# Kernel tuning notes

Measured on AMD Instinct MI355X. Metric: run time of the kernel, lower is better.

Reference implementation:

```python
import jax, jax.numpy as jnp
import numpy as np

L = 10
DIM = 4
TABLE = 1 << 16
BASE_RES = 16.0
PLS = 2.0
HID = 64
SCALE_MULTI = 0.5
DENSITY_OFFSET = -1.0
SCENE_SCALING = 2.0
PRIMES = (np.uint32(1), np.uint32(2654435761), np.uint32(805459861))


def _safe_exp(x):
    return jnp.exp(jnp.clip(x, -30.0, 10.0))


def _l2norm(x, eps=1e-8):
    return x / jnp.sqrt(jnp.sum(x * x, -1, keepdims=True) + eps)


def _circumcenters(tets):
    # tets: [T,4,3]; solve 2(vi-v0).c = |vi|^2-|v0|^2
    v0 = tets[:, 0]
    A = 2.0 * (tets[:, 1:] - v0[:, None, :]) + 1e-6 * jnp.eye(3, dtype=tets.dtype)
    b = jnp.sum(tets[:, 1:] ** 2, -1) - jnp.sum(v0 ** 2, -1)[:, None]
    c = jnp.linalg.solve(A, b[..., None])[..., 0]
    r = jnp.linalg.norm(c - v0, axis=-1)
    return c, r


def _project_to_tet(p, tets):
    # clamp-and-renormalize barycentric coordinates (approximate projection)
    v0 = tets[:, 0]
    E = tets[:, 1:] - v0[:, None, :]
    M = jnp.einsum('tid,tjd->tij', E, E) + 1e-6 * jnp.eye(3, dtype=tets.dtype)
    rhs = jnp.einsum('tid,td->ti', E, p - v0)
    lam = jnp.linalg.solve(M, rhs[..., None])[..., 0]
    bary = jnp.concatenate([1.0 - lam.sum(-1, keepdims=True), lam], -1)
    bary = jnp.clip(bary, 0.0, 1.0)
    bary = bary / jnp.clip(bary.sum(-1, keepdims=True), 1e-6, None)
    return jnp.einsum('tv,tvd->td', bary, tets)


def _contract_mean_std(x, std):
    # mipnerf-360 style scene contraction of mean; std scaled by |J| ~ 1/n^2
    n = jnp.maximum(jnp.linalg.norm(x, axis=-1, keepdims=True), 1e-9)
    cx = jnp.where(n <= 1.0, x, (2.0 - 1.0 / n) * x / n)
    cs = std * jnp.where(n[..., 0] <= 1.0, 1.0, 1.0 / (n[..., 0] ** 2))
    return cx, cs


def _hash_encode(pos, tables):
    # pos [T,3] in [0,1); tables [L, TABLE, DIM]; multiresolution hash grid
    mask = np.uint32(TABLE - 1)
    pos = jnp.clip(pos, 0.0, 1.0 - 1e-6)
    feats = []
    for l in range(L):
        res = float(np.floor(BASE_RES * (PLS ** l)))
        x = pos * res
        f = jnp.floor(x)
        w = x - f
        fi = f.astype(jnp.uint32)
        acc = jnp.zeros(pos.shape[:-1] + (DIM,), pos.dtype)
        for cz in (0, 1):
            for cy in (0, 1):
                for cx in (0, 1):
                    c = fi + jnp.asarray((cx, cy, cz), jnp.uint32)
                    h = ((c[..., 0] * PRIMES[0]) ^ (c[..., 1] * PRIMES[1]) ^ (c[..., 2] * PRIMES[2])) & mask
                    wt = ((w[..., 0] if cx else 1.0 - w[..., 0]) *
                          (w[..., 1] if cy else 1.0 - w[..., 1]) *
                          (w[..., 2] if cz else 1.0 - w[..., 2]))
                    acc = acc + tables[l][h.astype(jnp.int32)] * wt[..., None]
        feats.append(acc)
    return jnp.stack(feats, axis=1)  # [T, L, DIM]


def _forward(vertices, indices, center, tables, W1, b1, W2, b2, W3, b3):
    tets = vertices[indices]  # [T,4,3] gather
    cc, radius = _circumcenters(tets)
    cc = _project_to_tet(cc, tets)
    normalized = (cc - center) / SCENE_SCALING
    cv, cr = _contract_mean_std(normalized, radius / SCENE_SCALING)
    cr = cr * SCALE_MULTI
    n = jnp.arange(L, dtype=vertices.dtype)
    erf_x = 1.0 / jnp.sqrt(PLS * 4.0 * n[None, :] * cr[:, None] + 1e-12)
    scaling = jax.lax.erf(erf_x)  # [T, L] per-level erf anti-aliasing scale
    pos = cv * 0.25 + 0.5  # contracted [-2,2] -> [0,1]
    feats = _hash_encode(pos, tables) * scaling[..., None]
    h = feats.reshape(feats.shape[0], L * DIM)
    h = jax.nn.selu(h @ W1 + b1)
    h = jax.nn.selu(h @ W2 + b2)
    out = h @ W3 + b3  # [T, 13]
    density = _safe_exp(out[:, 0] + DENSITY_OFFSET)
    pairs = ((0, 1), (0, 2), (0, 3), (1, 2), (1, 3), (2, 3))
    el = jnp.stack([jnp.linalg.norm(tets[:, i] - tets[:, j], axis=1) for i, j in pairs], 0).max(0)
    alpha = 1.0 - jnp.exp(-density * el)
    V = vertices.shape[0]
    vertex_alpha = jnp.zeros((V,), vertices.dtype).at[indices].max(
        jnp.broadcast_to(alpha[:, None], indices.shape))  # scatter amax
    fs = out[:, 1:]
    base = fs[:, :3] + 0.5
    grads = jnp.clip(base[:, :, None], 0.0, None) * jnp.tanh(fs[:, 3:12].reshape(-1, 3, 3))
    offs = _l2norm(tets - cc[:, None, :])
    vcol = base[:, None, :] + jnp.einsum('tcd,tvd->tvc', grads, offs)  # [T,4,3]
    return vertex_alpha, vcol


def setup_inputs() -> dict:
    key = jax.random.key(0)
    ks = jax.random.split(key, 8)
    V, T = 100000, 500000
    vertices = jax.random.normal(ks[0], (V, 3), jnp.float32) * 0.5
    indices = jax.random.randint(ks[1], (T, 4), 0, V, jnp.int32)
    center = jnp.zeros((1, 3), jnp.float32)
    tables = jax.random.normal(ks[2], (L, TABLE, DIM), jnp.float32) * 1e-2
    def lin(k, i, o):
        s = (6.0 / (i + o)) ** 0.5
        return jax.random.uniform(k, (i, o), jnp.float32, -s, s)
    return dict(vertices=vertices, indices=indices, center=center, tables=tables,
                W1=lin(ks[3], L * DIM, HID), b1=jnp.zeros((HID,), jnp.float32),
                W2=lin(ks[4], HID, HID), b2=jnp.zeros((HID,), jnp.float32),
                W3=lin(ks[5], HID, 13), b3=jnp.zeros((13,), jnp.float32))


def reference(vertices, indices, center, tables, W1, b1, W2, b2, W3, b3):
    return _forward(vertices, indices, center, tables, W1, b1, W2, b2, W3, b3)
```

## Files before the change

kernel.cpp:

```cpp
#include <hip/hip_runtime.h>
#include <math.h>

#define NLVL 10
#define TBL 65536
#define NHID 64
#define NIN 40
#define LDP 68

typedef __attribute__((ext_vector_type(8))) short bf16x8;
typedef __attribute__((ext_vector_type(4))) float f32x4;
typedef unsigned int uint;

__device__ __forceinline__ float selu_f(float x) {
    return 1.0507009873554805f * (x > 0.0f ? x : 1.6732632423543772f * (__expf(x) - 1.0f));
}
__device__ __forceinline__ float fast_tanh(float x) {
    float xx = fminf(fmaxf(x, -15.0f), 15.0f);
    float t = __expf(2.0f * xx);
    return (t - 1.0f) / (t + 1.0f);
}
__device__ __forceinline__ unsigned short f2bf(float x) {
    unsigned u = __float_as_uint(x);
    unsigned r = (u + 0x7FFFu + ((u >> 16) & 1u)) >> 16;
    return (unsigned short)r;
}
__device__ __forceinline__ float bf2f(unsigned short h) {
    return __uint_as_float(((unsigned)h) << 16);
}
__device__ __forceinline__ short2 split_bf(float x) {
    unsigned short h = f2bf(x);
    float r = x - bf2f(h);
    short2 s;
    s.x = (short)h;
    s.y = (short)f2bf(r);
    return s;
}

__device__ __forceinline__ void solve3d(const double A[3][3], const double b[3], double x[3]) {
    double a00=A[0][0], a01=A[0][1], a02=A[0][2];
    double a10=A[1][0], a11=A[1][1], a12=A[1][2];
    double a20=A[2][0], a21=A[2][1], a22=A[2][2];
    double C00 =  (a11*a22 - a12*a21);
    double C01 = -(a10*a22 - a12*a20);
    double C02 =  (a10*a21 - a11*a20);
    double C10 = -(a01*a22 - a02*a21);
    double C11 =  (a00*a22 - a02*a20);
    double C12 = -(a00*a21 - a01*a20);
    double C20 =  (a01*a12 - a02*a11);
    double C21 = -(a00*a12 - a02*a10);
    double C22 =  (a00*a11 - a01*a10);
    double det = a00*C00 + a01*C01 + a02*C02;
    double inv = 1.0 / det;
    x[0] = (C00*b[0] + C10*b[1] + C20*b[2]) * inv;
    x[1] = (C01*b[0] + C11*b[1] + C21*b[2]) * inv;
    x[2] = (C02*b[0] + C12*b[1] + C22*b[2]) * inv;
}

__global__ void __launch_bounds__(256) zero_alpha_kernel(float* out, int V) {
    int i = blockIdx.x * blockDim.x + threadIdx.x;
    if (i < V) out[i] = 0.0f;
}

__device__ __forceinline__ void enc2(const float4* __restrict__ tb4,
                                     float px, float py, float pz, float crf,
                                     int l0, float f[8]) {
    uint idx[2][8];
    float wt[2][8];
    #pragma unroll
    for (int h = 0; h < 2; ++h) {
        int l = l0 + h;
        float res = (float)(16 << l);
        float x0 = px*res, x1 = py*res, x2 = pz*res;
        float f0 = floorf(x0), f1 = floorf(x1), f2 = floorf(x2);
        float w0 = x0-f0, w1 = x1-f1, w2 = x2-f2;
        uint i0 = (uint)f0, i1 = (uint)f1, i2 = (uint)f2;
        #pragma unroll
        for (int cn = 0; cn < 8; ++cn) {
            uint cx = (uint)(cn & 1), cy = (uint)((cn >> 1) & 1), cz = (uint)((cn >> 2) & 1);
            idx[h][cn] = (((i0 + cx) * 1u) ^ ((i1 + cy) * 2654435761u) ^ ((i2 + cz) * 805459861u)) & 65535u;
            wt[h][cn] = (cx ? w0 : 1.0f - w0) * (cy ? w1 : 1.0f - w1) * (cz ? w2 : 1.0f - w2);
        }
    }
    float4 v[2][8];
    #pragma unroll
    for (int h = 0; h < 2; ++h)
        #pragma unroll
        for (int cn = 0; cn < 8; ++cn)
            v[h][cn] = tb4[(size_t)(l0+h)*TBL + idx[h][cn]];
    #pragma unroll
    for (int h = 0; h < 2; ++h) {
        float a0=0.f, a1=0.f, a2=0.f, a3=0.f;
        #pragma unroll
        for (int cn = 0; cn < 8; ++cn) {
            float w = wt[h][cn];
            a0 = fmaf(v[h][cn].x, w, a0);
            a1 = fmaf(v[h][cn].y, w, a1);
            a2 = fmaf(v[h][cn].z, w, a2);
            a3 = fmaf(v[h][cn].w, w, a3);
        }
        float sc = erff(rsqrtf(8.0f*(float)(l0+h)*crf + 1e-12f));
        f[h*4+0] = a0*sc; f[h*4+1] = a1*sc; f[h*4+2] = a2*sc; f[h*4+3] = a3*sc;
    }
}

__global__ void __launch_bounds__(256) geomhash_kernel(
    const float* __restrict__ vertices,
    const int*   __restrict__ indices,
    const float* __restrict__ center,
    const float* __restrict__ tables,
    float* __restrict__ aux,
    float* __restrict__ feats, int T)
{
    int t = blockIdx.x * blockDim.x + threadIdx.x;
    if (t >= T) return;

    double p[4][3];
    #pragma unroll
    for (int v = 0; v < 4; ++v) {
        int vid = indices[t*4+v];
        p[v][0] = (double)vertices[vid*3+0];
        p[v][1] = (double)vertices[vid*3+1];
        p[v][2] = (double)vertices[vid*3+2];
    }

    double A[3][3], bb[3];
    double v0sq = p[0][0]*p[0][0] + p[0][1]*p[0][1] + p[0][2]*p[0][2];
    #pragma unroll
    for (int i = 0; i < 3; ++i) {
        #pragma unroll
        for (int j = 0; j < 3; ++j)
            A[i][j] = 2.0*(p[i+1][j] - p[0][j]) + (i==j ? 1e-6 : 0.0);
        bb[i] = p[i+1][0]*p[i+1][0] + p[i+1][1]*p[i+1][1] + p[i+1][2]*p[i+1][2] - v0sq;
    }
    double c[3];
    solve3d(A, bb, c);
    double dx0 = c[0]-p[0][0], dy0 = c[1]-p[0][1], dz0 = c[2]-p[0][2];
    double radius = sqrt(dx0*dx0 + dy0*dy0 + dz0*dz0);

    double E[3][3];
    #pragma unroll
    for (int i = 0; i < 3; ++i)
        #pragma unroll
        for (int j = 0; j < 3; ++j)
            E[i][j] = p[i+1][j] - p[0][j];
    double M[3][3], rhs[3];
    #pragma unroll
    for (int i = 0; i < 3; ++i) {
        #pragma unroll
        for (int k = 0; k < 3; ++k)
            M[i][k] = E[i][0]*E[k][0] + E[i][1]*E[k][1] + E[i][2]*E[k][2] + (i==k ? 1e-6 : 0.0);
        rhs[i] = E[i][0]*dx0 + E[i][1]*dy0 + E[i][2]*dz0;
    }
    double lam[3];
    solve3d(M, rhs, lam);
    double bary[4];
    bary[0] = 1.0 - lam[0] - lam[1] - lam[2];
    bary[1] = lam[0]; bary[2] = lam[1]; bary[3] = lam[2];
    double bs = 0.0;
    #pragma unroll
    for (int v = 0; v < 4; ++v) {
        bary[v] = fmin(fmax(bary[v], 0.0), 1.0);
        bs += bary[v];
    }
    bs = fmax(bs, 1e-6);
    double cc[3];
    #pragma unroll
    for (int j = 0; j < 3; ++j)
        cc[j] = (bary[0]*p[0][j] + bary[1]*p[1][j] + bary[2]*p[2][j] + bary[3]*p[3][j]) / bs;

    double xv[3];
    xv[0] = (cc[0] - (double)center[0]) * 0.5;
    xv[1] = (cc[1] - (double)center[1]) * 0.5;
    xv[2] = (cc[2] - (double)center[2]) * 0.5;
    double nrm = sqrt(xv[0]*xv[0] + xv[1]*xv[1] + xv[2]*xv[2]);
    double n = fmax(nrm, 1e-9);
    double cv[3], cs;
    if (n <= 1.0) {
        cv[0]=xv[0]; cv[1]=xv[1]; cv[2]=xv[2];
        cs = radius * 0.5;
    } else {
        double f = (2.0 - 1.0/n) / n;
        cv[0]=xv[0]*f; cv[1]=xv[1]*f; cv[2]=xv[2]*f;
        cs = radius * 0.5 / (n*n);
    }
    float crf = (float)(cs * 0.5);

    float px = fminf(fmaxf((float)(cv[0]*0.25 + 0.5), 0.0f), 1.0f - 1e-6f);
    float py = fminf(fmaxf((float)(cv[1]*0.25 + 0.5), 0.0f), 1.0f - 1e-6f);
    float pz = fminf(fmaxf((float)(cv[2]*0.25 + 0.5), 0.0f), 1.0f - 1e-6f);

    float el = 0.0f;
    #pragma unroll
    for (int a = 0; a < 3; ++a)
        #pragma unroll
        for (int bq = a+1; bq < 4; ++bq) {
            float ddx = (float)(p[a][0]-p[bq][0]);
            float ddy = (float)(p[a][1]-p[bq][1]);
            float ddz = (float)(p[a][2]-p[bq][2]);
            el = fmaxf(el, sqrtf(ddx*ddx + ddy*ddy + ddz*ddz));
        }

    size_t st = (size_t)T;
    aux[4*st + t] = (float)cc[0];
    aux[5*st + t] = (float)cc[1];
    aux[6*st + t] = (float)cc[2];
    aux[7*st + t] = el;

    const float4* tb4 = reinterpret_cast<const float4*>(tables);
    float4* frow = reinterpret_cast<float4*>(feats + (size_t)t * NIN);
    #pragma unroll
    for (int b = 0; b < 5; ++b) {
        float f[8];
        enc2(tb4, px, py, pz, crf, 2*b, f);
        frow[2*b+0] = make_float4(f[0], f[1], f[2], f[3]);
        frow[2*b+1] = make_float4(f[4], f[5], f[6], f[7]);
    }
}

__global__ void __launch_bounds__(256, 2) mlp_mfma_kernel(
    const float* __restrict__ feats,
    const float* __restrict__ aux,
    const float* __restrict__ vertices,
    const int*   __restrict__ indices,
    const float* __restrict__ W1, const float* __restrict__ b1,
    const float* __restrict__ W2, const float* __restrict__ b2,
    const float* __restrict__ W3, const float* __restrict__ b3,
    float* __restrict__ out, int T, int V)
{
    __shared__ __align__(16) float hts[4][16][LDP];

    const int tid  = threadIdx.x;
    const int wid  = tid >> 6;
    const int lane = tid & 63;
    const int r    = lane & 15;
    const int g    = lane >> 4;

    bf16x8 w1h[2][4];
    bf16x8 w1l0[4];
    #pragma unroll
    for (int s = 0; s < 2; ++s)
        #pragma unroll
        for (int nt = 0; nt < 4; ++nt) {
            bf16x8 h, lo;
            #pragma unroll
            for (int j = 0; j < 8; ++j) {
                int k = s*32 + g*8 + j;
                float w = (k < NIN) ? W1[k*NHID + nt*16 + r] : 0.0f;
                short2 sp = split_bf(w);
                h[j] = sp.x; lo[j] = sp.y;
            }
            w1h[s][nt] = h;
            if (s == 0) w1l0[nt] = lo;
        }
    bf16x8 w2h[2][4], w2l[2][4];
    #pragma unroll
    for (int s = 0; s < 2; ++s)
        #pragma unroll
        for (int nt = 0; nt < 4; ++nt) {
            bf16x8 h, lo;
            #pragma unroll
            for (int j = 0; j < 8; ++j) {
                int k = s*32 + g*8 + j;
                float w = W2[k*NHID + nt*16 + r];
                short2 sp = split_bf(w);
                h[j] = sp.x; lo[j] = sp.y;
            }
            w2h[s][nt] = h; w2l[s][nt] = lo;
        }
    bf16x8 w3h[2], w3l[2];
    #pragma unroll
    for (int s = 0; s < 2; ++s) {
        bf16x8 h, lo;
        #pragma unroll
        for (int j = 0; j < 8; ++j) {
            int k = s*32 + g*8 + j;
            float w = (r < 13) ? W3[k*13 + r] : 0.0f;
            short2 sp = split_bf(w);
            h[j] = sp.x; lo[j] = sp.y;
        }
        w3h[s] = h; w3l[s] = lo;
    }
    float b1v[4], b2v[4];
    #pragma unroll
    for (int nt = 0; nt < 4; ++nt) { b1v[nt] = b1[nt*16 + r]; b2v[nt] = b2[nt*16 + r]; }
    float b3v = (r < 13) ? b3[r] : 0.0f;

    const size_t st = (size_t)T;
    const int nmt = (T + 15) >> 4;
    const int gw = blockIdx.x * 4 + wid;
    const int gstride = gridDim.x * 4;

    for (int mt = gw; mt < nmt; mt += gstride) {
        const int t0 = mt * 16;
        const int trow = t0 + r;
        const bool rowok = trow < T;

        bf16x8 ah0, al0, ah1;
        {
            const float4* fr4 = reinterpret_cast<const float4*>(feats + (size_t)trow * NIN);
            float4 z = make_float4(0.f,0.f,0.f,0.f);
            float4 u0 = rowok ? fr4[g*2+0] : z;
            float4 u1 = rowok ? fr4[g*2+1] : z;
            short2 sp;
            sp = split_bf(u0.x); ah0[0]=sp.x; al0[0]=sp.y;
            sp = split_bf(u0.y); ah0[1]=sp.x; al0[1]=sp.y;
            sp = split_bf(u0.z); ah0[2]=sp.x; al0[2]=sp.y;
            sp = split_bf(u0.w); ah0[3]=sp.x; al0[3]=sp.y;
            sp = split_bf(u1.x); ah0[4]=sp.x; al0[4]=sp.y;
            sp = split_bf(u1.y); ah0[5]=sp.x; al0[5]=sp.y;
            sp = split_bf(u1.z); ah0[6]=sp.x; al0[6]=sp.y;
            sp = split_bf(u1.w); ah0[7]=sp.x; al0[7]=sp.y;
            bool k1ok = rowok && (g == 0);
            float4 v0 = k1ok ? fr4[8] : z;
            float4 v1 = k1ok ? fr4[9] : z;
            ah1[0] = (short)f2bf(v0.x); ah1[1] = (short)f2bf(v0.y);
            ah1[2] = (short)f2bf(v0.z); ah1[3] = (short)f2bf(v0.w);
            ah1[4] = (short)f2bf(v1.x); ah1[5] = (short)f2bf(v1.y);
            ah1[6] = (short)f2bf(v1.z); ah1[7] = (short)f2bf(v1.w);
        }

        #pragma unroll
        for (int nt = 0; nt < 4; ++nt) {
            f32x4 acc = {0.f, 0.f, 0.f, 0.f};
            acc = __builtin_amdgcn_mfma_f32_16x16x32_bf16(ah0, w1h[0][nt], acc, 0, 0, 0);
            acc = __builtin_amdgcn_mfma_f32_16x16x32_bf16(ah0, w1l0[nt],  acc, 0, 0, 0);
            acc = __builtin_amdgcn_mfma_f32_16x16x32_bf16(al0, w1h[0][nt], acc, 0, 0, 0);
            acc = __builtin_amdgcn_mfma_f32_16x16x32_bf16(ah1, w1h[1][nt], acc, 0, 0, 0);
            #pragma unroll
            for (int q = 0; q < 4; ++q)
                hts[wid][g*4 + q][nt*16 + r] = selu_f(acc[q] + b1v[nt]);
        }
        asm volatile("s_waitcnt lgkmcnt(0)" ::: "memory");

        bf16x8 a2h[2], a2l[2];
        #pragma unroll
        for (int s = 0; s < 2; ++s) {
            float4 u0 = *reinterpret_cast<const float4*>(&hts[wid][r][s*32 + g*8]);
            float4 u1 = *reinterpret_cast<const float4*>(&hts[wid][r][s*32 + g*8 + 4]);
            bf16x8 h, lo;
            short2 sp;
            sp = split_bf(u0.x); h[0]=sp.x; lo[0]=sp.y;
            sp = split_bf(u0.y); h[1]=sp.x; lo[1]=sp.y;
            sp = split_bf(u0.z); h[2]=sp.x; lo[2]=sp.y;
            sp = split_bf(u0.w); h[3]=sp.x; lo[3]=sp.y;
            sp = split_bf(u1.x); h[4]=sp.x; lo[4]=sp.y;
            sp = split_bf(u1.y); h[5]=sp.x; lo[5]=sp.y;
            sp = split_bf(u1.z); h[6]=sp.x; lo[6]=sp.y;
            sp = split_bf(u1.w); h[7]=sp.x; lo[7]=sp.y;
            a2h[s] = h; a2l[s] = lo;
        }
        asm volatile("s_waitcnt lgkmcnt(0)" ::: "memory");
        float h2v[4][4];
        #pragma unroll
        for (int nt = 0; nt < 4; ++nt) {
            f32x4 acc = {0.f, 0.f, 0.f, 0.f};
            #pragma unroll
            for (int s = 0; s < 2; ++s) {
                acc = __builtin_amdgcn_mfma_f32_16x16x32_bf16(a2h[s], w2h[s][nt], acc, 0, 0, 0);
                acc = __builtin_amdgcn_mfma_f32_16x16x32_bf16(a2h[s], w2l[s][nt], acc, 0, 0, 0);
                acc = __builtin_amdgcn_mfma_f32_16x16x32_bf16(a2l[s], w2h[s][nt], acc, 0, 0, 0);
            }
            #pragma unroll
            for (int q = 0; q < 4; ++q) h2v[nt][q] = selu_f(acc[q] + b2v[nt]);
        }
        #pragma unroll
        for (int nt = 0; nt < 4; ++nt)
            #pragma unroll
            for (int q = 0; q < 4; ++q)
                hts[wid][g*4 + q][nt*16 + r] = h2v[nt][q];
        asm volatile("s_waitcnt lgkmcnt(0)" ::: "memory");

        bf16x8 a3h[2], a3l[2];
        #pragma unroll
        for (int s = 0; s < 2; ++s) {
            float4 u0 = *reinterpret_cast<const float4*>(&hts[wid][r][s*32 + g*8]);
            float4 u1 = *reinterpret_cast<const float4*>(&hts[wid][r][s*32 + g*8 + 4]);
            bf16x8 h, lo;
            short2 sp;
            sp = split_bf(u0.x); h[0]=sp.x; lo[0]=sp.y;
            sp = split_bf(u0.y); h[1]=sp.x; lo[1]=sp.y;
            sp = split_bf(u0.z); h[2]=sp.x; lo[2]=sp.y;
            sp = split_bf(u0.w); h[3]=sp.x; lo[3]=sp.y;
            sp = split_bf(u1.x); h[4]=sp.x; lo[4]=sp.y;
            sp = split_bf(u1.y); h[5]=sp.x; lo[5]=sp.y;
            sp = split_bf(u1.z); h[6]=sp.x; lo[6]=sp.y;
            sp = split_bf(u1.w); h[7]=sp.x; lo[7]=sp.y;
            a3h[s] = h; a3l[s] = lo;
        }
        asm volatile("s_waitcnt lgkmcnt(0)" ::: "memory");
        {
            f32x4 acc = {0.f, 0.f, 0.f, 0.f};
            #pragma unroll
            for (int s = 0; s < 2; ++s) {
                acc = __builtin_amdgcn_mfma_f32_16x16x32_bf16(a3h[s], w3h[s], acc, 0, 0, 0);
                acc = __builtin_amdgcn_mfma_f32_16x16x32_bf16(a3h[s], w3l[s], acc, 0, 0, 0);
                acc = __builtin_amdgcn_mfma_f32_16x16x32_bf16(a3l[s], w3h[s], acc, 0, 0, 0);
            }
            #pragma unroll
            for (int q = 0; q < 4; ++q)
                hts[wid][g*4 + q][r] = acc[q] + b3v;
        }
        asm volatile("s_waitcnt lgkmcnt(0)" ::: "memory");

        {
            int et = lane >> 2;
            int ev = lane & 3;
            int te = t0 + et;
            if (te < T) {
                const float* orow = hts[wid][et];
                float4 o0 = *reinterpret_cast<const float4*>(&orow[0]);
                float4 o1 = *reinterpret_cast<const float4*>(&orow[4]);
                float4 o2 = *reinterpret_cast<const float4*>(&orow[8]);
                float o12 = orow[12];

                float el  = aux[7*st + te];
                float cc0 = aux[4*st + te], cc1 = aux[5*st + te], cc2 = aux[6*st + te];

                float dv = fminf(fmaxf(o0.x - 1.0f, -30.0f), 10.0f);
                float density = __expf(dv);
                float alpha = 1.0f - __expf(-density * el);
                int ab = __float_as_int(alpha);
                int vid = indices[te*4 + ev];
                atomicMax((int*)out + vid, ab);

                float base0 = o0.y + 0.5f, base1 = o0.z + 0.5f, base2 = o0.w + 0.5f;
                float bc0 = fmaxf(base0, 0.0f), bc1 = fmaxf(base1, 0.0f), bc2 = fmaxf(base2, 0.0f);
                float g00 = bc0*fast_tanh(o1.x), g01 = bc0*fast_tanh(o1.y), g02 = bc0*fast_tanh(o1.z);
                float g10 = bc1*fast_tanh(o1.w), g11 = bc1*fast_tanh(o2.x), g12 = bc1*fast_tanh(o2.y);
                float g20 = bc2*fast_tanh(o2.z), g21 = bc2*fast_tanh(o2.w), g22 = bc2*fast_tanh(o12);

                float pxv = vertices[vid*3+0], pyv = vertices[vid*3+1], pzv = vertices[vid*3+2];
                float ox = pxv-cc0, oy = pyv-cc1, oz = pzv-cc2;
                float inv = rsqrtf(ox*ox + oy*oy + oz*oz + 1e-8f);
                float q0 = ox*inv, q1 = oy*inv, q2 = oz*inv;
                float* vout = out + V + (size_t)te * 12 + ev*3;
                vout[0] = base0 + g00*q0 + g01*q1 + g02*q2;
                vout[1] = base1 + g10*q0 + g11*q1 + g12*q2;
                vout[2] = base2 + g20*q0 + g21*q1 + g22*q2;
            }
        }
        asm volatile("s_waitcnt lgkmcnt(0)" ::: "memory");
    }
}

__global__ void __launch_bounds__(256) tet_forward_fused(
    const float* __restrict__ vertices,
    const int*   __restrict__ indices,
    const float* __restrict__ center,
    const float* __restrict__ tables,
    const float* __restrict__ W1, const float* __restrict__ b1,
    const float* __restrict__ W2, const float* __restrict__ b2,
    const float* __restrict__ W3, const float* __restrict__ b3,
    float* __restrict__ out, int T, int V)
{
    int t = blockIdx.x * blockDim.x + threadIdx.x;
    if (t >= T) return;

    double p[4][3];
    int vv[4];
    #pragma unroll
    for (int v = 0; v < 4; ++v) {
        vv[v] = indices[t*4+v];
        p[v][0] = (double)vertices[vv[v]*3+0];
        p[v][1] = (double)vertices[vv[v]*3+1];
        p[v][2] = (double)vertices[vv[v]*3+2];
    }
    double A[3][3], bb[3];
    double v0sq = p[0][0]*p[0][0] + p[0][1]*p[0][1] + p[0][2]*p[0][2];
    #pragma unroll
    for (int i = 0; i < 3; ++i) {
        #pragma unroll
        for (int j = 0; j < 3; ++j)
            A[i][j] = 2.0*(p[i+1][j] - p[0][j]) + (i==j ? 1e-6 : 0.0);
        bb[i] = p[i+1][0]*p[i+1][0] + p[i+1][1]*p[i+1][1] + p[i+1][2]*p[i+1][2] - v0sq;
    }
    double c[3];
    solve3d(A, bb, c);
    double dx0 = c[0]-p[0][0], dy0 = c[1]-p[0][1], dz0 = c[2]-p[0][2];
    double radius = sqrt(dx0*dx0 + dy0*dy0 + dz0*dz0);
    double E[3][3];
    #pragma unroll
    for (int i = 0; i < 3; ++i)
        #pragma unroll
        for (int j = 0; j < 3; ++j)
            E[i][j] = p[i+1][j] - p[0][j];
    double M[3][3], rhs[3];
    #pragma unroll
    for (int i = 0; i < 3; ++i) {
        #pragma unroll
        for (int k = 0; k < 3; ++k)
            M[i][k] = E[i][0]*E[k][0] + E[i][1]*E[k][1] + E[i][2]*E[k][2] + (i==k ? 1e-6 : 0.0);
        rhs[i] = E[i][0]*dx0 + E[i][1]*dy0 + E[i][2]*dz0;
    }
    double lam[3];
    solve3d(M, rhs, lam);
    double bary[4];
    bary[0] = 1.0 - lam[0] - lam[1] - lam[2];
    bary[1] = lam[0]; bary[2] = lam[1]; bary[3] = lam[2];
    double bs = 0.0;
    #pragma unroll
    for (int v = 0; v < 4; ++v) { bary[v] = fmin(fmax(bary[v], 0.0), 1.0); bs += bary[v]; }
    bs = fmax(bs, 1e-6);
    double cc[3];
    #pragma unroll
    for (int j = 0; j < 3; ++j)
        cc[j] = (bary[0]*p[0][j] + bary[1]*p[1][j] + bary[2]*p[2][j] + bary[3]*p[3][j]) / bs;
    double xv[3];
    xv[0] = (cc[0] - (double)center[0]) * 0.5;
    xv[1] = (cc[1] - (double)center[1]) * 0.5;
    xv[2] = (cc[2] - (double)center[2]) * 0.5;
    double nrm = sqrt(xv[0]*xv[0] + xv[1]*xv[1] + xv[2]*xv[2]);
    double n = fmax(nrm, 1e-9);
    double cv[3], cs;
    if (n <= 1.0) { cv[0]=xv[0]; cv[1]=xv[1]; cv[2]=xv[2]; cs = radius * 0.5; }
    else { double f = (2.0 - 1.0/n) / n; cv[0]=xv[0]*f; cv[1]=xv[1]*f; cv[2]=xv[2]*f; cs = radius * 0.5 / (n*n); }
    float crf = (float)(cs * 0.5);
    float pos0 = fminf(fmaxf((float)(cv[0]*0.25 + 0.5), 0.0f), 1.0f - 1e-6f);
    float pos1 = fminf(fmaxf((float)(cv[1]*0.25 + 0.5), 0.0f), 1.0f - 1e-6f);
    float pos2 = fminf(fmaxf((float)(cv[2]*0.25 + 0.5), 0.0f), 1.0f - 1e-6f);

    float h0[NIN];
    float res = 16.0f;
    #pragma unroll
    for (int l = 0; l < NLVL; ++l) {
        float x0 = pos0*res, x1 = pos1*res, x2 = pos2*res;
        float f0 = floorf(x0), f1 = floorf(x1), f2 = floorf(x2);
        float w0 = x0-f0, w1 = x1-f1, w2 = x2-f2;
        unsigned i0 = (unsigned)f0, i1 = (unsigned)f1, i2 = (unsigned)f2;
        float a0=0.f, a1=0.f, a2=0.f, a3=0.f;
        #pragma unroll
        for (int cn = 0; cn < 8; ++cn) {
            unsigned cx = (unsigned)(cn & 1), cy = (unsigned)((cn >> 1) & 1), cz = (unsigned)((cn >> 2) & 1);
            unsigned hh = ((i0 + cx) * 1u) ^ ((i1 + cy) * 2654435761u) ^ ((i2 + cz) * 805459861u);
            hh &= 65535u;
            float wt = (cx ? w0 : 1.0f - w0) * (cy ? w1 : 1.0f - w1) * (cz ? w2 : 1.0f - w2);
            const float4 tv = *reinterpret_cast<const float4*>(tables + ((size_t)l*TBL + hh)*4);
            a0 = fmaf(tv.x, wt, a0); a1 = fmaf(tv.y, wt, a1);
            a2 = fmaf(tv.z, wt, a2); a3 = fmaf(tv.w, wt, a3);
        }
        float sc = erff(rsqrtf(8.0f*(float)l*crf + 1e-12f));
        h0[l*4+0] = a0*sc; h0[l*4+1] = a1*sc; h0[l*4+2] = a2*sc; h0[l*4+3] = a3*sc;
        res *= 2.0f;
    }

    float h1[NHID];
    #pragma unroll
    for (int j = 0; j < NHID; ++j) h1[j] = b1[j];
    #pragma unroll
    for (int i = 0; i < NIN; ++i) {
        float hi = h0[i];
        #pragma unroll
        for (int j = 0; j < NHID; ++j) h1[j] = fmaf(hi, W1[i*NHID + j], h1[j]);
    }
    #pragma unroll
    for (int j = 0; j < NHID; ++j) h1[j] = selu_f(h1[j]);

    float o[13];
    #pragma unroll
    for (int k = 0; k < 13; ++k) o[k] = b3[k];
    #pragma unroll
    for (int half = 0; half < 2; ++half) {
        float h2h[32];
        #pragma unroll
        for (int jj = 0; jj < 32; ++jj) h2h[jj] = b2[half*32 + jj];
        #pragma unroll
        for (int i = 0; i < NHID; ++i) {
            float hi = h1[i];
            #pragma unroll
            for (int jj = 0; jj < 32; ++jj)
                h2h[jj] = fmaf(hi, W2[i*NHID + half*32 + jj], h2h[jj]);
        }
        #pragma unroll
        for (int jj = 0; jj < 32; ++jj) {
            float hv = selu_f(h2h[jj]);
            #pragma unroll
            for (int k = 0; k < 13; ++k)
                o[k] = fmaf(hv, W3[(half*32 + jj)*13 + k], o[k]);
        }
    }

    float dv = fminf(fmaxf(o[0] - 1.0f, -30.0f), 10.0f);
    float density = __expf(dv);
    float el = 0.0f;
    #pragma unroll
    for (int a = 0; a < 3; ++a)
        #pragma unroll
        for (int bq = a+1; bq < 4; ++bq) {
            float ddx = (float)(p[a][0]-p[bq][0]);
            float ddy = (float)(p[a][1]-p[bq][1]);
            float ddz = (float)(p[a][2]-p[bq][2]);
            el = fmaxf(el, sqrtf(ddx*ddx + ddy*ddy + ddz*ddz));
        }
    float alpha = 1.0f - __expf(-density * el);
    int ab = __float_as_int(alpha);
    atomicMax((int*)out + vv[0], ab);
    atomicMax((int*)out + vv[1], ab);
    atomicMax((int*)out + vv[2], ab);
    atomicMax((int*)out + vv[3], ab);

    float base0 = o[1] + 0.5f, base1 = o[2] + 0.5f, base2 = o[3] + 0.5f;
    float bc0 = fmaxf(base0, 0.0f), bc1 = fmaxf(base1, 0.0f), bc2 = fmaxf(base2, 0.0f);
    float g00 = bc0*fast_tanh(o[4]),  g01 = bc0*fast_tanh(o[5]),  g02 = bc0*fast_tanh(o[6]);
    float g10 = bc1*fast_tanh(o[7]),  g11 = bc1*fast_tanh(o[8]),  g12 = bc1*fast_tanh(o[9]);
    float g20 = bc2*fast_tanh(o[10]), g21 = bc2*fast_tanh(o[11]), g22 = bc2*fast_tanh(o[12]);

    float* vout = out + V + (size_t)t * 12;
    #pragma unroll
    for (int v = 0; v < 4; ++v) {
        float ox = (float)(p[v][0]-cc[0]), oy = (float)(p[v][1]-cc[1]), oz = (float)(p[v][2]-cc[2]);
        float inv = rsqrtf(ox*ox + oy*oy + oz*oz + 1e-8f);
        float q0 = ox*inv, q1 = oy*inv, q2 = oz*inv;
        vout[v*3+0] = base0 + g00*q0 + g01*q1 + g02*q2;
        vout[v*3+1] = base1 + g10*q0 + g11*q1 + g12*q2;
        vout[v*3+2] = base2 + g20*q0 + g21*q1 + g22*q2;
    }
}

extern "C" void kernel_launch(void* const* d_in, const int* in_sizes, int n_in,
                              void* d_out, int out_size, void* d_ws, size_t ws_size,
                              hipStream_t stream) {
    const float* vertices = (const float*)d_in[0];
    const int*   indices  = (const int*)d_in[1];
    const float* center   = (const float*)d_in[2];
    const float* tables   = (const float*)d_in[3];
    const float* W1 = (const float*)d_in[4];
    const float* b1 = (const float*)d_in[5];
    const float* W2 = (const float*)d_in[6];
    const float* b2 = (const float*)d_in[7];
    const float* W3 = (const float*)d_in[8];
    const float* b3 = (const float*)d_in[9];
    int V = in_sizes[0] / 3;
    int T = in_sizes[1] / 4;
    float* out = (float*)d_out;

    hipLaunchKernelGGL(zero_alpha_kernel, dim3((V + 255) / 256), dim3(256), 0, stream, out, V);

    size_t need = (size_t)T * 48 * sizeof(float);
    dim3 grid((T + 255) / 256), blk(256);
    if (ws_size >= need) {
        float* aux   = (float*)d_ws;
        float* feats = aux + (size_t)T * 8;
        hipLaunchKernelGGL(geomhash_kernel, grid, blk, 0, stream,
                           vertices, indices, center, tables, aux, feats, T);
        hipLaunchKernelGGL(mlp_mfma_kernel, dim3(512), blk, 0, stream, feats, aux, vertices, indices,
                           W1, b1, W2, b2, W3, b3, out, T, V);
    } else {
        hipLaunchKernelGGL(tet_forward_fused, grid, blk, 0, stream,
                           vertices, indices, center, tables, W1, b1, W2, b2, W3, b3, out, T, V);
    }
}
```

Before: 252.1 us.

## Split hash encoding into per-level-pair passes for table cache locality

The geometry kernel now encodes only levels 0-1 and stores the contracted position and cone radius into aux. Four extra kernels each encode one pair of levels. The aim is to keep each pass's two hash tables (about 2 MB) resident in cache instead of scattering gathers across all ten tables at once. The MLP kernel grid is also doubled to 1024 blocks. In exchange the passes add kernel launches, re-read aux, and write feats with strided partial stores.

```diff
diff --git a/kernel.cpp b/kernel.cpp
--- a/kernel.cpp
+++ b/kernel.cpp
@@ -103,7 +103,7 @@
     }
 }
 
-__global__ void __launch_bounds__(256) geomhash_kernel(
+__global__ void __launch_bounds__(256) geom01_kernel(
     const float* __restrict__ vertices,
     const int*   __restrict__ indices,
     const float* __restrict__ center,
@@ -201,6 +201,10 @@
         }
 
     size_t st = (size_t)T;
+    aux[0*st + t] = px;
+    aux[1*st + t] = py;
+    aux[2*st + t] = pz;
+    aux[3*st + t] = crf;
     aux[4*st + t] = (float)cc[0];
     aux[5*st + t] = (float)cc[1];
     aux[6*st + t] = (float)cc[2];
@@ -208,13 +212,32 @@
 
     const float4* tb4 = reinterpret_cast<const float4*>(tables);
     float4* frow = reinterpret_cast<float4*>(feats + (size_t)t * NIN);
-    #pragma unroll
-    for (int b = 0; b < 5; ++b) {
-        float f[8];
-        enc2(tb4, px, py, pz, crf, 2*b, f);
-        frow[2*b+0] = make_float4(f[0], f[1], f[2], f[3]);
-        frow[2*b+1] = make_float4(f[4], f[5], f[6], f[7]);
-    }
+    float f01[8];
+    enc2(tb4, px, py, pz, crf, 0, f01);
+    frow[0] = make_float4(f01[0], f01[1], f01[2], f01[3]);
+    frow[1] = make_float4(f01[4], f01[5], f01[6], f01[7]);
+}
+
+template<int L0>
+__global__ void __launch_bounds__(256) hash_pass_kernel(
+    const float* __restrict__ tables,
+    const float* __restrict__ aux,
+    float* __restrict__ feats, int T)
+{
+    int t = blockIdx.x * blockDim.x + threadIdx.x;
+    if (t >= T) return;
+    size_t st = (size_t)T;
+    float px = aux[0*st + t];
+    float py = aux[1*st + t];
+    float pz = aux[2*st + t];
+    float crf = aux[3*st + t];
+    const float4* tb4 = reinterpret_cast<const float4*>(tables);
+    float4* frow = reinterpret_cast<float4*>(feats + (size_t)t * NIN);
+
+    float f[8];
+    enc2(tb4, px, py, pz, crf, L0, f);
+    frow[L0]     = make_float4(f[0], f[1], f[2], f[3]);
+    frow[L0 + 1] = make_float4(f[4], f[5], f[6], f[7]);
 }
 
 __global__ void __launch_bounds__(256, 2) mlp_mfma_kernel(
@@ -640,9 +663,13 @@
     if (ws_size >= need) {
         float* aux   = (float*)d_ws;
         float* feats = aux + (size_t)T * 8;
-        hipLaunchKernelGGL(geomhash_kernel, grid, blk, 0, stream,
+        hipLaunchKernelGGL(geom01_kernel, grid, blk, 0, stream,
                            vertices, indices, center, tables, aux, feats, T);
-        hipLaunchKernelGGL(mlp_mfma_kernel, dim3(512), blk, 0, stream, feats, aux, vertices, indices,
+        hipLaunchKernelGGL((hash_pass_kernel<2>), grid, blk, 0, stream, tables, aux, feats, T);
+        hipLaunchKernelGGL((hash_pass_kernel<4>), grid, blk, 0, stream, tables, aux, feats, T);
+        hipLaunchKernelGGL((hash_pass_kernel<6>), grid, blk, 0, stream, tables, aux, feats, T);
+        hipLaunchKernelGGL((hash_pass_kernel<8>), grid, blk, 0, stream, tables, aux, feats, T);
+        hipLaunchKernelGGL(mlp_mfma_kernel, dim3(1024), blk, 0, stream, feats, aux, vertices, indices,
                            W1, b1, W2, b2, W3, b3, out, T, V);
     } else {
         hipLaunchKernelGGL(tet_forward_fused, grid, blk, 0, stream,
```

Result: faster. 237.7 us (-5.7%).
